# Kernel tuning notes

Hardware: AMD Instinct MI355X
Metric: run time of the kernel (lower is better)

The kernel has to match this reference:

```python
import jax, jax.numpy as jnp
import numpy as np

N, R, E = 20000, 4, 40000
C_IN, C_EDGE, HID, OUT = 256, 128, 512, 256
H = 8
D = HID // H
SCALE = 1.0 / float(np.sqrt(D))


def _hgt_layer(x, src, dst, Wkqv, bkqv, Wk, Wv, prel, Wout, bout, skip):
    # x: [n, c_in]; src/dst: [R, E] int; Wk/Wv: [R, H, D, D]; prel: [R, H]
    n = x.shape[0]
    kqv = x @ Wkqv + bkqv                      # [n, 3*HID], split order k|q|v (torch.tensor_split)
    k, q, v = jnp.split(kqv, 3, axis=1)
    k = k.reshape(n, H, D)
    q = q.reshape(n, H, D)
    v = v.reshape(n, H, D)
    # per-(relation, head) DxD transforms (HeteroLinear k_rel / v_rel, no bias)
    k_rel = jnp.einsum('nhd,rhde->rnhe', k, Wk)   # [R, n, H, D]
    v_rel = jnp.einsum('nhd,rhde->rnhe', v, Wv)
    gather = jax.vmap(lambda t, i: t[i])          # per-relation gather
    k_e = gather(k_rel, src)                      # [R, E, H, D]
    v_e = gather(v_rel, src)
    q_e = q[dst]                                  # [R, E, H, D]
    alpha = jnp.einsum('rehd,rehd->reh', q_e, k_e) * prel[:, None, :] * SCALE
    m = src.shape[0] * src.shape[1]
    alpha = alpha.reshape(m, H)
    dstf = dst.reshape(m)
    # segment softmax over destination nodes, jointly across all relations
    amax = jax.ops.segment_max(alpha, dstf, num_segments=n)      # [n, H]
    ae = jnp.exp(alpha - amax[dstf])
    denom = jax.ops.segment_sum(ae, dstf, num_segments=n)
    w = ae / (denom[dstf] + 1e-16)
    msg = (v_e.reshape(m, H, D) * w[:, :, None]).reshape(m, H * D)
    agg = jax.ops.segment_sum(msg, dstf, num_segments=n)          # [n, HID]
    out = jax.nn.gelu(agg, approximate=False) @ Wout + bout
    if skip is not None:  # sigmoid-gated residual, only when dims match
        a = jax.nn.sigmoid(skip)
        out = a * out + (1.0 - a) * x
    return out


def setup_inputs() -> dict:
    key = jax.random.key(0)
    ks = jax.random.split(key, 16)
    def g(k, shape, fan):
        return jax.random.normal(k, shape, jnp.float32) / np.sqrt(fan)
    inp = {
        'x': jax.random.normal(ks[0], (N, C_IN), jnp.float32),
        'edge_index': jax.random.randint(ks[1], (R, 2, E), 0, N),
        'edge_attr': jax.random.normal(ks[2], (R, E, C_EDGE), jnp.float32),
        'Wkqv0': g(ks[3], (C_IN, 3 * HID), C_IN), 'bkqv0': jnp.zeros((3 * HID,), jnp.float32),
        'Wk0': g(ks[4], (R, H, D, D), D), 'Wv0': g(ks[5], (R, H, D, D), D),
        'prel0': jnp.ones((R, H), jnp.float32),
        'Wout0': g(ks[6], (HID, HID), HID), 'bout0': jnp.zeros((HID,), jnp.float32),
        'Wkqv1': g(ks[7], (HID, 3 * HID), HID), 'bkqv1': jnp.zeros((3 * HID,), jnp.float32),
        'Wk1': g(ks[8], (R, H, D, D), D), 'Wv1': g(ks[9], (R, H, D, D), D),
        'prel1': jnp.ones((R, H), jnp.float32),
        'Wout1': g(ks[10], (HID, HID), HID), 'bout1': jnp.zeros((HID,), jnp.float32),
        'skip1': jnp.ones((), jnp.float32),
        'Wfc': g(ks[11], (HID, OUT), HID), 'bfc': jnp.zeros((OUT,), jnp.float32),
        'We1': g(ks[12], (C_EDGE, HID), C_EDGE), 'be1': jnp.zeros((HID,), jnp.float32),
        'We2': g(ks[13], (HID, OUT), HID), 'be2': jnp.zeros((OUT,), jnp.float32),
    }
    return inp


def reference(x, edge_index, edge_attr, Wkqv0, bkqv0, Wk0, Wv0, prel0, Wout0, bout0, Wkqv1, bkqv1, Wk1, Wv1, prel1, Wout1, bout1, skip1, Wfc, bfc, We1, be1, We2, be2):
    src = edge_index[:, 0, :]
    dst = edge_index[:, 1, :]
    h = _hgt_layer(x, src, dst, Wkqv0, bkqv0, Wk0, Wv0, prel0, Wout0, bout0, None)
    h = _hgt_layer(h, src, dst, Wkqv1, bkqv1, Wk1, Wv1, prel1, Wout1, bout1, skip1)
    node_embeds = h @ Wfc + bfc
    e = edge_attr.reshape(R * E, C_EDGE)  # concat over relations
    edge_embeds = jax.nn.relu(e @ We1 + be1) @ We2 + be2
    return node_embeds, edge_embeds
```

## Files before the change

### kernel.cpp

```cpp
#include <hip/hip_runtime.h>
#include <cstdint>
#include <cstddef>

#define NN      20000
#define RR      4
#define EE      40000
#define CIN     256
#define CEDGE   128
#define HIDW    512
#define OUTW    256
#define NH      8
#define MEDGE   (RR*EE)
#define SCALEF  0.125f

typedef unsigned short u16;
typedef short s8v  __attribute__((ext_vector_type(8)));
typedef float f32x4 __attribute__((ext_vector_type(4)));

#define B_KQV   10240000ull
#define B_KREL  71680000ull
#define B_AGG   153600000ull
#define B_H0    174080000ull
#define B_H1    194560000ull
#define B_ALPHA 215040000ull
#define B_LSE   220160000ull
#define B_ROWP  220800000ull
#define B_EREC  220880128ull
#define B_WTS   221520128ull
#define WS_NEED 227000000ull

#define SZH ((size_t)NN * 256)

__device__ __forceinline__ u16 f2b(float f) {
    unsigned u = __float_as_uint(f);
    unsigned r = (u + 0x7FFFu + ((u >> 16) & 1u)) >> 16;
    return (u16)r;
}
__device__ __forceinline__ float b2f(u16 h) { return __uint_as_float(((unsigned)h) << 16); }
__device__ __forceinline__ float gelu_exact(float x) {
    return 0.5f * x * (1.0f + erff(x * 0.70710678118654752f));
}

__device__ __forceinline__ void gl_lds16(const u16* g, u16* l) {
    __builtin_amdgcn_global_load_lds(
        (const __attribute__((address_space(1))) void*)g,
        (__attribute__((address_space(3))) void*)l, 16, 0, 0);
}

template<int BN, int ACT, bool OUTBF16, bool BIAS, bool SKIP, bool AF32 = false>
__global__ __launch_bounds__(256) void gemm_bf16(
    const void* __restrict__ Av, int lda, size_t astride,
    const u16* __restrict__ BT, int ldb, size_t bstride,
    const float* __restrict__ bias,
    void* __restrict__ Cv, int ldc, size_t cstride,
    int M, int K,
    const u16* __restrict__ skipx, const float* __restrict__ gatep)
{
    constexpr int FN = BN / 32;
    constexpr int BI = BN / 32;
    __shared__ __align__(16) u16 As[128 * 64];
    __shared__ __align__(16) u16 Bs[BN * 64];

    const int t = threadIdx.x, lane = t & 63, wid = t >> 6;
    const int m0 = blockIdx.y * 128, n0 = blockIdx.x * BN;
    const int z  = blockIdx.z;
    const u16*   Bz = BT + (size_t)z * bstride;
    const float* Af = (const float*)Av + (AF32 ? (size_t)z * astride : 0);
    const u16*   Au = (const u16*)Av   + (AF32 ? 0 : (size_t)z * astride);
    const int wm = wid >> 1, wn = wid & 1;

    const int srow   = lane >> 3;
    const int schunk = (lane & 7) ^ srow;

    f32x4 acc[4][FN];
    #pragma unroll
    for (int i = 0; i < 4; ++i)
        #pragma unroll
        for (int j = 0; j < FN; ++j)
            acc[i][j] = (f32x4){0.f, 0.f, 0.f, 0.f};

    for (int k0 = 0; k0 < K; k0 += 64) {
        if (AF32) {
            #pragma unroll
            for (int i = 0; i < 4; ++i) {
                int c = i * 256 + t;
                int row = c >> 3, cc = c & 7;
                int gr = m0 + row; gr = gr < M ? gr : M - 1;
                const float* Ap = Af + (size_t)gr * lda + k0 + cc * 8;
                float4 p = *(const float4*)Ap;
                float4 q = *(const float4*)(Ap + 4);
                s8v v;
                v[0] = (short)f2b(p.x); v[1] = (short)f2b(p.y);
                v[2] = (short)f2b(p.z); v[3] = (short)f2b(p.w);
                v[4] = (short)f2b(q.x); v[5] = (short)f2b(q.y);
                v[6] = (short)f2b(q.z); v[7] = (short)f2b(q.w);
                *(s8v*)&As[row * 64 + ((cc ^ (row & 7)) << 3)] = v;
            }
        } else {
            #pragma unroll
            for (int i = 0; i < 4; ++i) {
                int t4 = wid * 4 + i;
                int row = t4 * 8 + srow;
                int gr = m0 + row; gr = gr < M ? gr : M - 1;
                gl_lds16(Au + (size_t)gr * lda + k0 + schunk * 8, &As[t4 * 512]);
            }
        }
        #pragma unroll
        for (int i = 0; i < BI; ++i) {
            int tb = wid * BI + i;
            int col = n0 + tb * 8 + srow;
            gl_lds16(Bz + (size_t)col * ldb + k0 + schunk * 8, &Bs[tb * 512]);
        }
        __syncthreads();
        #pragma unroll
        for (int ks = 0; ks < 2; ++ks) {
            s8v af[4], bf[FN];
            #pragma unroll
            for (int i = 0; i < 4; ++i) {
                int arow = wm * 64 + i * 16 + (lane & 15);
                int ac   = (ks * 4 + (lane >> 4)) ^ (lane & 7);
                af[i] = *(const s8v*)&As[arow * 64 + ac * 8];
            }
            #pragma unroll
            for (int j = 0; j < FN; ++j) {
                int brow = wn * (BN / 2) + j * 16 + (lane & 15);
                int bc   = (ks * 4 + (lane >> 4)) ^ (lane & 7);
                bf[j] = *(const s8v*)&Bs[brow * 64 + bc * 8];
            }
            #pragma unroll
            for (int i = 0; i < 4; ++i)
                #pragma unroll
                for (int j = 0; j < FN; ++j)
                    acc[i][j] = __builtin_amdgcn_mfma_f32_16x16x32_bf16(af[i], bf[j], acc[i][j], 0, 0, 0);
        }
        __syncthreads();
    }

    float gate = 1.f, ogate = 0.f;
    if (SKIP) { float s = *gatep; gate = 1.f / (1.f + expf(-s)); ogate = 1.f - gate; }
    u16*   Cb = (u16*)Cv   + (size_t)z * cstride;
    float* Cf = (float*)Cv + (size_t)z * cstride;
    #pragma unroll
    for (int i = 0; i < 4; ++i) {
        int rbase = m0 + wm * 64 + i * 16 + (lane >> 4) * 4;
        #pragma unroll
        for (int j = 0; j < FN; ++j) {
            int col = n0 + wn * (BN / 2) + j * 16 + (lane & 15);
            float bv = BIAS ? bias[col] : 0.f;
            #pragma unroll
            for (int q = 0; q < 4; ++q) {
                int r = rbase + q;
                if (r >= M) continue;
                float v = acc[i][j][q] + bv;
                if (ACT == 1) v = fmaxf(v, 0.f);
                if (ACT == 2) v = gelu_exact(v);
                if (SKIP) v = gate * v + ogate * b2f(skipx[(size_t)r * ldc + col]);
                if (OUTBF16) Cb[(size_t)r * ldc + col] = f2b(v);
                else         Cf[(size_t)r * ldc + col] = v;
            }
        }
    }
}

__global__ __launch_bounds__(512) void edge_mlp(
    const float* __restrict__ ea, const u16* __restrict__ We1T,
    const float* __restrict__ b1, const u16* __restrict__ We2T,
    const float* __restrict__ b2, float* __restrict__ out)
{
    __shared__ __align__(16) u16 Ae[128 * 128];
    __shared__ __align__(16) u16 Ic[128 * 128];

    const int t = threadIdx.x, lane = t & 63, w = t >> 6;
    const int e0 = blockIdx.x * 128;
    const int l15 = lane & 15, l4 = lane >> 4;

    s8v w1f[4];
    auto loadW1 = [&](s8v* dst, int c) {
        #pragma unroll
        for (int ks = 0; ks < 4; ++ks) {
            int col1 = c * 128 + w * 16 + l15;
            dst[ks] = *(const s8v*)(We1T + (size_t)col1 * 128 + ks * 32 + l4 * 8);
        }
    };
    loadW1(w1f, 0);

    #pragma unroll
    for (int i = 0; i < 8; ++i) {
        int f   = i * 512 + t;
        int row = f >> 5;
        int c4  = f & 31;
        float4 p = *(const float4*)(ea + (size_t)(e0 + row) * 128 + c4 * 4);
        unsigned lo = (unsigned)f2b(p.x) | ((unsigned)f2b(p.y) << 16);
        unsigned hi = (unsigned)f2b(p.z) | ((unsigned)f2b(p.w) << 16);
        int chunk = c4 >> 1;
        int sub   = (c4 & 1) * 8;
        *(uint2*)((char*)Ae + row * 256 + ((chunk ^ (row & 7)) << 4) + sub)
            = make_uint2(lo, hi);
    }
    __syncthreads();

    f32x4 acc2[8][2];
    #pragma unroll
    for (int m = 0; m < 8; ++m) {
        acc2[m][0] = (f32x4){0.f, 0.f, 0.f, 0.f};
        acc2[m][1] = (f32x4){0.f, 0.f, 0.f, 0.f};
    }

    #pragma unroll
    for (int c = 0; c < 4; ++c) {
        f32x4 sacc[8];
        #pragma unroll
        for (int m = 0; m < 8; ++m) sacc[m] = (f32x4){0.f, 0.f, 0.f, 0.f};
        #pragma unroll
        for (int ks = 0; ks < 4; ++ks) {
            #pragma unroll
            for (int m = 0; m < 8; ++m) {
                int row = m * 16 + l15;
                int kc  = (ks * 4 + l4) ^ (row & 7);
                s8v af = *(const s8v*)&Ae[row * 128 + kc * 8];
                sacc[m] = __builtin_amdgcn_mfma_f32_16x16x32_bf16(af, w1f[ks], sacc[m], 0, 0, 0);
            }
        }
        s8v w2f[4][2];
        #pragma unroll
        for (int ks = 0; ks < 4; ++ks)
            #pragma unroll
            for (int n = 0; n < 2; ++n) {
                int col = w * 32 + n * 16 + l15;
                w2f[ks][n] = *(const s8v*)(We2T + (size_t)col * 512 + c * 128 + ks * 32 + l4 * 8);
            }
        __syncthreads();
        {
            int col = w * 16 + l15;
            float bv = b1[c * 128 + col];
            int chunk = col >> 3, sub = col & 7;
            #pragma unroll
            for (int m = 0; m < 8; ++m)
                #pragma unroll
                for (int q = 0; q < 4; ++q) {
                    int row = m * 16 + l4 * 4 + q;
                    float v = fmaxf(sacc[m][q] + bv, 0.f);
                    Ic[row * 128 + ((chunk ^ (row & 7)) << 3) + sub] = f2b(v);
                }
        }
        if (c < 3) loadW1(w1f, c + 1);
        __syncthreads();
        #pragma unroll
        for (int ks = 0; ks < 4; ++ks) {
            #pragma unroll
            for (int m = 0; m < 8; ++m) {
                int row = m * 16 + l15;
                int kc  = (ks * 4 + l4) ^ (row & 7);
                s8v af = *(const s8v*)&Ic[row * 128 + kc * 8];
                acc2[m][0] = __builtin_amdgcn_mfma_f32_16x16x32_bf16(af, w2f[ks][0], acc2[m][0], 0, 0, 0);
                acc2[m][1] = __builtin_amdgcn_mfma_f32_16x16x32_bf16(af, w2f[ks][1], acc2[m][1], 0, 0, 0);
            }
        }
    }

    #pragma unroll
    for (int n = 0; n < 2; ++n) {
        int col = w * 32 + n * 16 + l15;
        float bv = b2[col];
        #pragma unroll
        for (int m = 0; m < 8; ++m)
            #pragma unroll
            for (int q = 0; q < 4; ++q) {
                int row = m * 16 + l4 * 4 + q;
                out[(size_t)(e0 + row) * 256 + col] = acc2[m][n][q] + bv;
            }
    }
}

__global__ __launch_bounds__(256) void transpose_f2b(
    const float* __restrict__ W, u16* __restrict__ WT, int K, int N)
{
    __shared__ float tile[32][33];
    int kb = blockIdx.x * 32, nb = blockIdx.y * 32;
    int tx = threadIdx.x & 31, ty = threadIdx.x >> 5;
    #pragma unroll
    for (int i = 0; i < 32; i += 8)
        tile[ty + i][tx] = W[(size_t)(kb + ty + i) * N + nb + tx];
    __syncthreads();
    #pragma unroll
    for (int i = 0; i < 32; i += 8)
        WT[(size_t)(nb + ty + i) * K + kb + tx] = f2b(tile[tx][ty + i]);
}

__global__ void conv_wk(const float* __restrict__ Wk, u16* __restrict__ WkT)
{
    int idx = blockIdx.x * 256 + threadIdx.x;
    if (idx >= 8 * 256 * 64) return;
    int d = idx & 63, re = (idx >> 6) & 255, h = idx >> 14;
    int e = re & 63, r = re >> 6;
    WkT[idx] = f2b(Wk[(size_t)(((r * 8 + h) * 64 + d) * 64) + e]);
}

__global__ void conv_wv(const float* __restrict__ Wv, u16* __restrict__ WvT)
{
    int idx = blockIdx.x * 256 + threadIdx.x;
    if (idx >= 8 * 64 * 256) return;
    int d = idx & 63, r = (idx >> 6) & 3, e = (idx >> 8) & 63, h = idx >> 14;
    WvT[idx] = f2b(Wv[(size_t)(((r * 8 + h) * 64 + d) * 64) + e]);
}

__global__ void deg_kernel(const int* __restrict__ ei, int* __restrict__ rowptr)
{
    int idx = blockIdx.x * 256 + threadIdx.x;
    if (idx >= MEDGE) return;
    int r = idx / EE;
    atomicAdd(&rowptr[ei[idx + (r + 1) * EE]], 1);
}

__global__ __launch_bounds__(256) void scan_kernel(int* __restrict__ rowptr)
{
    __shared__ int buf[256];
    __shared__ int carry;
    const int t = threadIdx.x;
    if (t == 0) carry = 0;
    __syncthreads();
    for (int base = 0; base < NN; base += 256) {
        int i = base + t;
        int v = (i < NN) ? rowptr[i] : 0;
        buf[t] = v;
        __syncthreads();
        for (int off = 1; off < 256; off <<= 1) {
            int tv = (t >= off) ? buf[t - off] : 0;
            __syncthreads();
            buf[t] += tv;
            __syncthreads();
        }
        int total = buf[255];
        int excl = buf[t] - v;
        int c = carry;
        __syncthreads();
        if (i < NN) rowptr[i] = c + excl;
        if (t == 0) carry = c + total;
        __syncthreads();
    }
    if (t == 0) rowptr[NN] = carry;
}

__global__ void fill_kernel(const int* __restrict__ ei, const int* __restrict__ rowptr,
                            int* __restrict__ fillcnt, int* __restrict__ erec)
{
    int idx = blockIdx.x * 256 + threadIdx.x;
    if (idx >= MEDGE) return;
    int r = idx / EE;
    int dst = ei[idx + (r + 1) * EE];
    int pos = rowptr[dst] + atomicAdd(&fillcnt[dst], 1);
    erec[pos] = idx;
}

__global__ __launch_bounds__(256) void alpha_stats(
    const u16* __restrict__ krel2, const u16* __restrict__ kqvb,
    const int* __restrict__ ei, const int* __restrict__ rowptr,
    const int* __restrict__ erec, const float* __restrict__ prel,
    float* __restrict__ alpha, float* __restrict__ lse)
{
    int n    = (blockIdx.x * 256 + threadIdx.x) >> 6;
    int lane = threadIdx.x & 63;
    if (n >= NN) return;
    int p0 = rowptr[n], p1 = rowptr[n + 1];
    int h = lane >> 3, sub = lane & 7;
    s8v qv = *(const s8v*)(kqvb + (size_t)n * 1536 + 512 + h * 64 + sub * 8);
    float qf[8];
    #pragma unroll
    for (int q = 0; q < 8; ++q) qf[q] = b2f((u16)qv[q]);
    float m = -3.0e38f, ssum = 0.f;
    for (int j = p0; j < p1; ++j) {
        int idx = erec[j];
        int r = idx / EE;
        int src = ei[idx + r * EE];
        s8v kv = *(const s8v*)(krel2 + (size_t)src * 2048 + h * 256 + r * 64 + sub * 8);
        float s = 0.f;
        #pragma unroll
        for (int q = 0; q < 8; ++q) s += b2f((u16)kv[q]) * qf[q];
        s += __shfl_xor(s, 1);
        s += __shfl_xor(s, 2);
        s += __shfl_xor(s, 4);
        float a = s * prel[r * NH + h] * SCALEF;
        if (sub == 0) alpha[(size_t)idx * 8 + h] = a;
        float mn = fmaxf(m, a);
        ssum = ssum * expf(m - mn) + expf(a - mn);
        m = mn;
    }
    if (sub == 0) lse[(size_t)n * 8 + h] = m + logf(ssum + 1e-16f);
}

__global__ __launch_bounds__(256) void wsum_all(
    const u16* __restrict__ kqvb, const float* __restrict__ alpha,
    const float* __restrict__ lse, const int* __restrict__ rowptr,
    const int* __restrict__ erec, const int* __restrict__ ei,
    u16* __restrict__ wsumH)
{
    int n    = (blockIdx.x * 256 + threadIdx.x) >> 6;
    int lane = threadIdx.x & 63;
    if (n >= NN) return;
    int p0 = rowptr[n], p1 = rowptr[n + 1];
    int h = lane >> 3;
    float ls = lse[(size_t)n * 8 + h];
    float a0[8] = {}, a1[8] = {}, a2[8] = {}, a3[8] = {};
    for (int j = p0; j < p1; ++j) {
        int idx = erec[j];
        int r = idx / EE;
        int src = ei[idx + r * EE];
        float w = expf(alpha[(size_t)idx * 8 + h] - ls);
        s8v vv = *(const s8v*)(kqvb + (size_t)src * 1536 + 1024 + lane * 8);
        if (r == 0) {
            #pragma unroll
            for (int q = 0; q < 8; ++q) a0[q] += w * b2f((u16)vv[q]);
        } else if (r == 1) {
            #pragma unroll
            for (int q = 0; q < 8; ++q) a1[q] += w * b2f((u16)vv[q]);
        } else if (r == 2) {
            #pragma unroll
            for (int q = 0; q < 8; ++q) a2[q] += w * b2f((u16)vv[q]);
        } else {
            #pragma unroll
            for (int q = 0; q < 8; ++q) a3[q] += w * b2f((u16)vv[q]);
        }
    }
    u16* base = wsumH + (size_t)h * SZH + (size_t)n * 256 + (lane & 7) * 8;
    s8v o;
    #pragma unroll
    for (int q = 0; q < 8; ++q) o[q] = (short)f2b(a0[q]);
    *(s8v*)(base + 0)   = o;
    #pragma unroll
    for (int q = 0; q < 8; ++q) o[q] = (short)f2b(a1[q]);
    *(s8v*)(base + 64)  = o;
    #pragma unroll
    for (int q = 0; q < 8; ++q) o[q] = (short)f2b(a2[q]);
    *(s8v*)(base + 128) = o;
    #pragma unroll
    for (int q = 0; q < 8; ++q) o[q] = (short)f2b(a3[q]);
    *(s8v*)(base + 192) = o;
}

extern "C" void kernel_launch(void* const* d_in, const int* in_sizes, int n_in,
                              void* d_out, int out_size, void* d_ws, size_t ws_size,
                              hipStream_t stream)
{
    const float* x    = (const float*)d_in[0];
    const int*   ei   = (const int*)d_in[1];
    const float* ea   = (const float*)d_in[2];
    const float* Wkqv[2] = {(const float*)d_in[3],  (const float*)d_in[10]};
    const float* bkqv[2] = {(const float*)d_in[4],  (const float*)d_in[11]};
    const float* Wk[2]   = {(const float*)d_in[5],  (const float*)d_in[12]};
    const float* Wv[2]   = {(const float*)d_in[6],  (const float*)d_in[13]};
    const float* prel[2] = {(const float*)d_in[7],  (const float*)d_in[14]};
    const float* Wout[2] = {(const float*)d_in[8],  (const float*)d_in[15]};
    const float* bout[2] = {(const float*)d_in[9],  (const float*)d_in[16]};
    const float* skip1 = (const float*)d_in[17];
    const float* Wfc   = (const float*)d_in[18];
    const float* bfc   = (const float*)d_in[19];
    const float* We1   = (const float*)d_in[20];
    const float* be1   = (const float*)d_in[21];
    const float* We2   = (const float*)d_in[22];
    const float* be2   = (const float*)d_in[23];

    if (ws_size < WS_NEED) return;

    char* wsb = (char*)d_ws;
    u16*   kqvb  = (u16*)(wsb + B_KQV);
    u16*   krel2 = (u16*)(wsb + B_KREL);
    u16*   wsumH = krel2;
    u16*   aggb  = (u16*)(wsb + B_AGG);
    u16*   h0b   = (u16*)(wsb + B_H0);
    u16*   h1b   = (u16*)(wsb + B_H1);
    float* alpha = (float*)(wsb + B_ALPHA);
    float* lse   = (float*)(wsb + B_LSE);
    int*   fillcnt = (int*)(wsb + B_LSE);
    int*   rowptr  = (int*)(wsb + B_ROWP);
    int*   erec    = (int*)(wsb + B_EREC);
    float* outf  = (float*)d_out;

    u16* wt = (u16*)(wsb + B_WTS);
    u16* WkqvT[2] = {wt, wt + 393216};              wt += 393216 + 786432;
    u16* WkT[2]   = {wt, wt + 131072};              wt += 262144;
    u16* WvT[2]   = {wt, wt + 131072};              wt += 262144;
    u16* WoutT[2] = {wt, wt + 262144};              wt += 524288;
    u16* WfcT     = wt;                             wt += 131072;
    u16* We1T     = wt;                             wt += 65536;
    u16* We2T     = wt;

    const dim3 blk(256);
    const int mt128  = (NN + 127) / 128;

    transpose_f2b<<<dim3(CIN / 32, 1536 / 32), blk, 0, stream>>>(Wkqv[0], WkqvT[0], CIN, 1536);
    transpose_f2b<<<dim3(HIDW / 32, 1536 / 32), blk, 0, stream>>>(Wkqv[1], WkqvT[1], HIDW, 1536);
    transpose_f2b<<<dim3(HIDW / 32, HIDW / 32), blk, 0, stream>>>(Wout[0], WoutT[0], HIDW, HIDW);
    transpose_f2b<<<dim3(HIDW / 32, HIDW / 32), blk, 0, stream>>>(Wout[1], WoutT[1], HIDW, HIDW);
    transpose_f2b<<<dim3(HIDW / 32, OUTW / 32), blk, 0, stream>>>(Wfc, WfcT, HIDW, OUTW);
    transpose_f2b<<<dim3(CEDGE / 32, HIDW / 32), blk, 0, stream>>>(We1, We1T, CEDGE, HIDW);
    transpose_f2b<<<dim3(HIDW / 32, OUTW / 32), blk, 0, stream>>>(We2, We2T, HIDW, OUTW);
    for (int l = 0; l < 2; ++l) {
        conv_wk<<<(131072 + 255) / 256, blk, 0, stream>>>(Wk[l], WkT[l]);
        conv_wv<<<(131072 + 255) / 256, blk, 0, stream>>>(Wv[l], WvT[l]);
    }

    hipMemsetAsync(rowptr, 0, (NN + 1) * sizeof(int), stream);
    hipMemsetAsync(fillcnt, 0, NN * sizeof(int), stream);
    deg_kernel<<<(MEDGE + 255) / 256, blk, 0, stream>>>(ei, rowptr);
    scan_kernel<<<1, blk, 0, stream>>>(rowptr);
    fill_kernel<<<(MEDGE + 255) / 256, blk, 0, stream>>>(ei, rowptr, fillcnt, erec);

    for (int l = 0; l < 2; ++l) {
        int K = (l == 0) ? CIN : HIDW;

        if (l == 0)
            gemm_bf16<128, 0, true, true, false, true><<<dim3(12, mt128), blk, 0, stream>>>(
                (const void*)x, K, 0, WkqvT[0], K, 0, bkqv[0], kqvb, 1536, 0, NN, K, nullptr, nullptr);
        else
            gemm_bf16<128, 0, true, true, false><<<dim3(12, mt128), blk, 0, stream>>>(
                (const void*)h0b, K, 0, WkqvT[1], K, 0, bkqv[1], kqvb, 1536, 0, NN, K, nullptr, nullptr);

        gemm_bf16<128, 0, true, false, false><<<dim3(2, mt128, NH), blk, 0, stream>>>(
            (const void*)kqvb, 1536, 64, WkT[l], 64, (size_t)256 * 64, nullptr,
            krel2, 2048, 256, NN, 64, nullptr, nullptr);

        alpha_stats<<<(NN * 64) / 256, blk, 0, stream>>>(
            krel2, kqvb, ei, rowptr, erec, prel[l], alpha, lse);

        wsum_all<<<(NN * 64) / 256, blk, 0, stream>>>(
            kqvb, alpha, lse, rowptr, erec, ei, wsumH);

        gemm_bf16<64, 2, true, false, false><<<dim3(1, mt128, NH), blk, 0, stream>>>(
            (const void*)wsumH, 256, SZH, WvT[l], 256, (size_t)64 * 256, nullptr,
            aggb, 512, 64, NN, 256, nullptr, nullptr);

        if (l == 0)
            gemm_bf16<128, 0, true, true, false><<<dim3(4, mt128), blk, 0, stream>>>(
                (const void*)aggb, 512, 0, WoutT[0], 512, 0, bout[0], h0b, 512, 0, NN, 512, nullptr, nullptr);
        else
            gemm_bf16<128, 0, true, true, true><<<dim3(4, mt128), blk, 0, stream>>>(
                (const void*)aggb, 512, 0, WoutT[1], 512, 0, bout[1], h1b, 512, 0, NN, 512, h0b, skip1);
    }

    gemm_bf16<128, 0, false, true, false><<<dim3(2, mt128), blk, 0, stream>>>(
        (const void*)h1b, 512, 0, WfcT, 512, 0, bfc, outf, 256, 0, NN, 512, nullptr, nullptr);

    edge_mlp<<<MEDGE / 128, dim3(512), 0, stream>>>(ea, We1T, be1, We2T, be2, outf + 5120000);
}
```

Measured before the change: 762.6 us.

## Fold relation key transform into per-destination query and fuse attention kernels

Instead of projecting every source node's key through the per-relation matrix (k_rel), the query of each destination node is multiplied by the transposed relation matrices, so the gather reads raw keys from the kqv buffer. The alpha/log-sum-exp pass and the weighted value sum are fused into one kernel that computes the softmax normaliser in registers, which drops the lse round trip and one launch. The weighted sums are written in place over the per-node qW buffer, and the value GEMM's strides are changed to match. In-place aliasing is only safe because each warp reads its own node's qW row before overwriting it.

After: 775.4 us. No clear change (+1.7%).

```diff
diff --git a/kernel.cpp b/kernel.cpp
--- a/kernel.cpp
+++ b/kernel.cpp
@@ -28,8 +28,6 @@
 #define B_EREC  220880128ull
 #define B_WTS   221520128ull
 #define WS_NEED 227000000ull
-
-#define SZH ((size_t)NN * 256)
 
 __device__ __forceinline__ u16 f2b(float f) {
     unsigned u = __float_as_uint(f);
@@ -287,13 +285,13 @@
         WT[(size_t)(nb + ty + i) * K + kb + tx] = f2b(tile[tx][ty + i]);
 }
 
-__global__ void conv_wk(const float* __restrict__ Wk, u16* __restrict__ WkT)
+__global__ void conv_wk2(const float* __restrict__ Wk, u16* __restrict__ WkT2)
 {
     int idx = blockIdx.x * 256 + threadIdx.x;
     if (idx >= 8 * 256 * 64) return;
-    int d = idx & 63, re = (idx >> 6) & 255, h = idx >> 14;
-    int e = re & 63, r = re >> 6;
-    WkT[idx] = f2b(Wk[(size_t)(((r * 8 + h) * 64 + d) * 64) + e]);
+    int e = idx & 63, rd = (idx >> 6) & 255, h = idx >> 14;
+    int d = rd & 63, r = rd >> 6;
+    WkT2[idx] = f2b(Wk[(size_t)(((r * 8 + h) * 64 + d) * 64) + e]);
 }
 
 __global__ void conv_wv(const float* __restrict__ Wv, u16* __restrict__ WvT)
@@ -352,54 +350,70 @@
     erec[pos] = idx;
 }
 
-__global__ __launch_bounds__(256) void alpha_stats(
-    const u16* __restrict__ krel2, const u16* __restrict__ kqvb,
+__global__ __launch_bounds__(256) void gather_attn(
+    const u16* __restrict__ kqvb, const u16* __restrict__ qW,
     const int* __restrict__ ei, const int* __restrict__ rowptr,
     const int* __restrict__ erec, const float* __restrict__ prel,
-    float* __restrict__ alpha, float* __restrict__ lse)
+    float* __restrict__ alpha, u16* __restrict__ wsum2)
 {
     int n    = (blockIdx.x * 256 + threadIdx.x) >> 6;
     int lane = threadIdx.x & 63;
     if (n >= NN) return;
     int p0 = rowptr[n], p1 = rowptr[n + 1];
     int h = lane >> 3, sub = lane & 7;
-    s8v qv = *(const s8v*)(kqvb + (size_t)n * 1536 + 512 + h * 64 + sub * 8);
-    float qf[8];
-    #pragma unroll
-    for (int q = 0; q < 8; ++q) qf[q] = b2f((u16)qv[q]);
+
+    float qf0[8], qf1[8], qf2[8], qf3[8];
+    {
+        const u16* qp = qW + (size_t)n * 2048 + h * 256 + sub * 8;
+        s8v v0 = *(const s8v*)(qp + 0);
+        s8v v1 = *(const s8v*)(qp + 64);
+        s8v v2 = *(const s8v*)(qp + 128);
+        s8v v3 = *(const s8v*)(qp + 192);
+        #pragma unroll
+        for (int q = 0; q < 8; ++q) {
+            qf0[q] = b2f((u16)v0[q]); qf1[q] = b2f((u16)v1[q]);
+            qf2[q] = b2f((u16)v2[q]); qf3[q] = b2f((u16)v3[q]);
+        }
+    }
+    float pr0 = prel[0 * NH + h] * SCALEF, pr1 = prel[1 * NH + h] * SCALEF;
+    float pr2 = prel[2 * NH + h] * SCALEF, pr3 = prel[3 * NH + h] * SCALEF;
+
     float m = -3.0e38f, ssum = 0.f;
     for (int j = p0; j < p1; ++j) {
         int idx = erec[j];
         int r = idx / EE;
         int src = ei[idx + r * EE];
-        s8v kv = *(const s8v*)(krel2 + (size_t)src * 2048 + h * 256 + r * 64 + sub * 8);
+        s8v kv = *(const s8v*)(kqvb + (size_t)src * 1536 + h * 64 + sub * 8);
         float s = 0.f;
-        #pragma unroll
-        for (int q = 0; q < 8; ++q) s += b2f((u16)kv[q]) * qf[q];
-        s += __shfl_xor(s, 1);
-        s += __shfl_xor(s, 2);
-        s += __shfl_xor(s, 4);
-        float a = s * prel[r * NH + h] * SCALEF;
+        float a;
+        if (r == 0) {
+            #pragma unroll
+            for (int q = 0; q < 8; ++q) s += b2f((u16)kv[q]) * qf0[q];
+            s += __shfl_xor(s, 1); s += __shfl_xor(s, 2); s += __shfl_xor(s, 4);
+            a = s * pr0;
+        } else if (r == 1) {
+            #pragma unroll
+            for (int q = 0; q < 8; ++q) s += b2f((u16)kv[q]) * qf1[q];
+            s += __shfl_xor(s, 1); s += __shfl_xor(s, 2); s += __shfl_xor(s, 4);
+            a = s * pr1;
+        } else if (r == 2) {
+            #pragma unroll
+            for (int q = 0; q < 8; ++q) s += b2f((u16)kv[q]) * qf2[q];
+            s += __shfl_xor(s, 1); s += __shfl_xor(s, 2); s += __shfl_xor(s, 4);
+            a = s * pr2;
+        } else {
+            #pragma unroll
+            for (int q = 0; q < 8; ++q) s += b2f((u16)kv[q]) * qf3[q];
+            s += __shfl_xor(s, 1); s += __shfl_xor(s, 2); s += __shfl_xor(s, 4);
+            a = s * pr3;
+        }
         if (sub == 0) alpha[(size_t)idx * 8 + h] = a;
         float mn = fmaxf(m, a);
         ssum = ssum * expf(m - mn) + expf(a - mn);
         m = mn;
     }
-    if (sub == 0) lse[(size_t)n * 8 + h] = m + logf(ssum + 1e-16f);
-}
-
-__global__ __launch_bounds__(256) void wsum_all(
-    const u16* __restrict__ kqvb, const float* __restrict__ alpha,
-    const float* __restrict__ lse, const int* __restrict__ rowptr,
-    const int* __restrict__ erec, const int* __restrict__ ei,
-    u16* __restrict__ wsumH)
-{
-    int n    = (blockIdx.x * 256 + threadIdx.x) >> 6;
-    int lane = threadIdx.x & 63;
-    if (n >= NN) return;
-    int p0 = rowptr[n], p1 = rowptr[n + 1];
-    int h = lane >> 3;
-    float ls = lse[(size_t)n * 8 + h];
+    float ls = m + logf(ssum + 1e-16f);
+
     float a0[8] = {}, a1[8] = {}, a2[8] = {}, a3[8] = {};
     for (int j = p0; j < p1; ++j) {
         int idx = erec[j];
@@ -421,7 +435,7 @@
             for (int q = 0; q < 8; ++q) a3[q] += w * b2f((u16)vv[q]);
         }
     }
-    u16* base = wsumH + (size_t)h * SZH + (size_t)n * 256 + (lane & 7) * 8;
+    u16* base = wsum2 + (size_t)n * 2048 + h * 256 + (lane & 7) * 8;
     s8v o;
     #pragma unroll
     for (int q = 0; q < 8; ++q) o[q] = (short)f2b(a0[q]);
@@ -463,13 +477,11 @@
 
     char* wsb = (char*)d_ws;
     u16*   kqvb  = (u16*)(wsb + B_KQV);
-    u16*   krel2 = (u16*)(wsb + B_KREL);
-    u16*   wsumH = krel2;
+    u16*   qWbuf = (u16*)(wsb + B_KREL);
     u16*   aggb  = (u16*)(wsb + B_AGG);
     u16*   h0b   = (u16*)(wsb + B_H0);
     u16*   h1b   = (u16*)(wsb + B_H1);
     float* alpha = (float*)(wsb + B_ALPHA);
-    float* lse   = (float*)(wsb + B_LSE);
     int*   fillcnt = (int*)(wsb + B_LSE);
     int*   rowptr  = (int*)(wsb + B_ROWP);
     int*   erec    = (int*)(wsb + B_EREC);
@@ -477,7 +489,7 @@
 
     u16* wt = (u16*)(wsb + B_WTS);
     u16* WkqvT[2] = {wt, wt + 393216};              wt += 393216 + 786432;
-    u16* WkT[2]   = {wt, wt + 131072};              wt += 262144;
+    u16* WkT2[2]  = {wt, wt + 131072};              wt += 262144;
     u16* WvT[2]   = {wt, wt + 131072};              wt += 262144;
     u16* WoutT[2] = {wt, wt + 262144};              wt += 524288;
     u16* WfcT     = wt;                             wt += 131072;
@@ -495,7 +507,7 @@
     transpose_f2b<<<dim3(CEDGE / 32, HIDW / 32), blk, 0, stream>>>(We1, We1T, CEDGE, HIDW);
     transpose_f2b<<<dim3(HIDW / 32, OUTW / 32), blk, 0, stream>>>(We2, We2T, HIDW, OUTW);
     for (int l = 0; l < 2; ++l) {
-        conv_wk<<<(131072 + 255) / 256, blk, 0, stream>>>(Wk[l], WkT[l]);
+        conv_wk2<<<(131072 + 255) / 256, blk, 0, stream>>>(Wk[l], WkT2[l]);
         conv_wv<<<(131072 + 255) / 256, blk, 0, stream>>>(Wv[l], WvT[l]);
     }
 
@@ -516,17 +528,14 @@
                 (const void*)h0b, K, 0, WkqvT[1], K, 0, bkqv[1], kqvb, 1536, 0, NN, K, nullptr, nullptr);
 
         gemm_bf16<128, 0, true, false, false><<<dim3(2, mt128, NH), blk, 0, stream>>>(
-            (const void*)kqvb, 1536, 64, WkT[l], 64, (size_t)256 * 64, nullptr,
-            krel2, 2048, 256, NN, 64, nullptr, nullptr);
-
-        alpha_stats<<<(NN * 64) / 256, blk, 0, stream>>>(
-            krel2, kqvb, ei, rowptr, erec, prel[l], alpha, lse);
-
-        wsum_all<<<(NN * 64) / 256, blk, 0, stream>>>(
-            kqvb, alpha, lse, rowptr, erec, ei, wsumH);
+            (const void*)(kqvb + 512), 1536, 64, WkT2[l], 64, (size_t)256 * 64, nullptr,
+            qWbuf, 2048, 256, NN, 64, nullptr, nullptr);
+
+        gather_attn<<<(NN * 64) / 256, blk, 0, stream>>>(
+            kqvb, qWbuf, ei, rowptr, erec, prel[l], alpha, qWbuf);
 
         gemm_bf16<64, 2, true, false, false><<<dim3(1, mt128, NH), blk, 0, stream>>>(
-            (const void*)wsumH, 256, SZH, WvT[l], 256, (size_t)64 * 256, nullptr,
+            (const void*)qWbuf, 2048, 256, WvT[l], 256, (size_t)64 * 256, nullptr,
             aggb, 512, 64, NN, 256, nullptr, nullptr);
 
         if (l == 0)
```
